# Optimization experiments

Hardware: AMD Instinct MI355X
Metric: run time of the kernel (lower is better)

## Reference

```python
import jax, jax.numpy as jnp
import numpy as np

N = 1024
E = 10
IN = 78
NOTE = 128
BEAT = 64
MEAS = 32
S = NOTE + (BEAT + MEAS) * 2  # 320, GatedGraph state width
SEC = NOTE                    # secondary_size
HEADS = 8
NPB = 4    # notes per beat
BPM = 4    # beats per measure
NB = N // NPB                 # 256 beats
NM = N // (NPB * BPM)         # 64 measures
SEQ_ITER = 2
GRAPH_ITER = 2


def setup_inputs() -> dict:
    key = jax.random.key(0)
    ks = iter(jax.random.split(key, 64))
    def rn(shape, s=0.05):
        return jax.random.normal(next(ks), shape, jnp.float32) * s
    nodes = jax.random.normal(next(ks), (1, N, IN), jnp.float32)
    adjacency = (jax.random.uniform(next(ks), (E, N, N)) < 0.01).astype(jnp.float32)
    beat_numbers = jnp.arange(N, dtype=jnp.int32) // NPB
    measure_numbers = jnp.arange(N, dtype=jnp.int32) // (NPB * BPM)
    inp = dict(nodes=nodes, adjacency=adjacency,
               beat_numbers=beat_numbers, measure_numbers=measure_numbers,
               num_beats=NB, num_measures=NM)
    inp['note_fc_w'] = rn((IN, NOTE)); inp['note_fc_b'] = rn((NOTE,))
    for g in ('g1', 'g2'):
        inp[g+'_wz'] = rn((E, S, SEC)); inp[g+'_wr'] = rn((E, S, SEC)); inp[g+'_wh'] = rn((E, S, SEC))
        inp[g+'_uz'] = rn((SEC, SEC)); inp[g+'_ur'] = rn((SEC, SEC)); inp[g+'_uh'] = rn((SEC, SEC))
        inp[g+'_bz'] = rn((SEC,)); inp[g+'_br'] = rn((SEC,)); inp[g+'_bh'] = rn((SEC,))
    inp['gb_w'] = rn((S, S)); inp['gb_b'] = rn((S,))
    inp['batt_w'] = rn((2*NOTE, 2*NOTE)); inp['batt_b'] = rn((2*NOTE,)); inp['batt_c'] = rn((HEADS, 2*NOTE//HEADS), 1.0)
    inp['matt_w'] = rn((2*BEAT, 2*BEAT)); inp['matt_b'] = rn((2*BEAT,)); inp['matt_c'] = rn((HEADS, 2*BEAT//HEADS), 1.0)
    inp['blstm_wi_f'] = rn((4*BEAT, 2*NOTE)); inp['blstm_wh_f'] = rn((4*BEAT, BEAT)); inp['blstm_b_f'] = rn((4*BEAT,))
    inp['blstm_wi_b'] = rn((4*BEAT, 2*NOTE)); inp['blstm_wh_b'] = rn((4*BEAT, BEAT)); inp['blstm_b_b'] = rn((4*BEAT,))
    inp['mlstm_wi_f'] = rn((4*MEAS, 2*BEAT)); inp['mlstm_wh_f'] = rn((4*MEAS, MEAS)); inp['mlstm_b_f'] = rn((4*MEAS,))
    inp['mlstm_wi_b'] = rn((4*MEAS, 2*BEAT)); inp['mlstm_wh_b'] = rn((4*MEAS, MEAS)); inp['mlstm_b_b'] = rn((4*MEAS,))
    return inp


def gated_graph(x, adj, wz, wr, wh, uz, ur, uh, bz, br, bh, n_iter, sec):
    # x: (N, S); adj: (E, N, N). Faithful to virtuosoNet GatedGraph (batch=1).
    for _ in range(n_iter):
        act = jnp.einsum('emn,mf->enf', adj, x)            # adj[e]^T @ x
        mz = jnp.einsum('enf,efs->ns', act, wz)            # sum over edge types
        mr = jnp.einsum('enf,efs->ns', act, wr)
        mh = jnp.einsum('enf,efs->ns', act, wh)
        xs = x[:, -sec:]
        z = jax.nn.sigmoid(mz + xs @ uz + bz)
        r = jax.nn.sigmoid(mr + xs @ ur + br)
        h = jnp.tanh(mh + (r * xs) @ uh + bh)
        new_sec = (1.0 - z) * xs + r * h                   # virtuosoNet update rule
        x = jnp.concatenate([x[:, :-sec], new_sec], axis=1)
    return x


def seg_attention(x, seg, G, W, b, c):
    # ContextAttention pooled per ragged segment. x: (M, D), c: (H, hd)
    M, D = x.shape
    H, hd = c.shape
    a = jnp.tanh(x @ W + b).reshape(M, H, hd)
    sim = jnp.einsum('mhd,hd->mh', a, c)
    mx = jax.ops.segment_max(sim, seg, num_segments=G)
    w = jnp.exp(sim - mx[seg])
    den = jax.ops.segment_sum(w, seg, num_segments=G)
    w = w / den[seg]
    out = jax.ops.segment_sum(x.reshape(M, H, hd) * w[:, :, None], seg, num_segments=G)
    return out.reshape(G, D)


def lstm_dir(x, wi, wh, b, H):
    def step(carry, xt):
        h, c = carry
        g = wi @ xt + wh @ h + b
        i, f, gg, o = jnp.split(g, 4)
        c = jax.nn.sigmoid(f) * c + jax.nn.sigmoid(i) * jnp.tanh(gg)
        h = jax.nn.sigmoid(o) * jnp.tanh(c)
        return (h, c), h
    init = (jnp.zeros((H,), x.dtype), jnp.zeros((H,), x.dtype))
    _, hs = jax.lax.scan(step, init, x)
    return hs


def bilstm(x, wif, whf, bf, wib, whb, bb, H):
    fw = lstm_dir(x, wif, whf, bf, H)
    bw = lstm_dir(x[::-1], wib, whb, bb, H)[::-1]
    return jnp.concatenate([fw, bw], axis=-1)


def reference(nodes, adjacency, note_fc_w, note_fc_b,
              g1_wz, g1_wr, g1_wh, g1_uz, g1_ur, g1_uh, g1_bz, g1_br, g1_bh,
              gb_w, gb_b,
              g2_wz, g2_wr, g2_wh, g2_uz, g2_ur, g2_uh, g2_bz, g2_br, g2_bh,
              batt_w, batt_b, batt_c, matt_w, matt_b, matt_c,
              blstm_wi_f, blstm_wh_f, blstm_b_f, blstm_wi_b, blstm_wh_b, blstm_b_b,
              mlstm_wi_f, mlstm_wh_f, mlstm_b_f, mlstm_wi_b, mlstm_wh_b, mlstm_b_b,
              beat_numbers, measure_numbers, num_beats, num_measures):
    n = nodes.shape[1]
    x0 = jnp.tanh(nodes[0] @ note_fc_w + note_fc_b)                     # (N, NOTE)
    notes_hidden = jnp.concatenate(
        [jnp.zeros((n, (BEAT + MEAS) * 2), jnp.float32), x0], axis=1)  # (N, S)
    # measure index of each beat = measure at the first note of that beat
    beat_to_meas = jax.ops.segment_min(measure_numbers, beat_numbers, num_segments=num_beats)
    nh2 = notes_hidden
    for _ in range(SEQ_ITER):
        nh = gated_graph(notes_hidden, adjacency, g1_wz, g1_wr, g1_wh,
                         g1_uz, g1_ur, g1_uh, g1_bz, g1_br, g1_bh, GRAPH_ITER, SEC)
        nb = jax.nn.relu(nh @ gb_w + gb_b)
        nh2 = gated_graph(nb, adjacency, g2_wz, g2_wr, g2_wh,
                          g2_uz, g2_ur, g2_uh, g2_bz, g2_br, g2_bh, GRAPH_ITER, SEC)
        cat = jnp.concatenate([nh[:, -SEC:], nh2[:, -SEC:]], axis=-1)   # (N, 2*NOTE)
        beat_nodes = seg_attention(cat, beat_numbers, num_beats, batt_w, batt_b, batt_c)
        beat_hidden = bilstm(beat_nodes, blstm_wi_f, blstm_wh_f, blstm_b_f,
                             blstm_wi_b, blstm_wh_b, blstm_b_b, BEAT)   # (NB, 2*BEAT)
        measure_nodes = seg_attention(beat_hidden, beat_to_meas, num_measures, matt_w, matt_b, matt_c)
        measure_hidden = bilstm(measure_nodes, mlstm_wi_f, mlstm_wh_f, mlstm_b_f,
                                mlstm_wi_b, mlstm_wh_b, mlstm_b_b, MEAS)  # (NM, 2*MEAS)
        beat_spanned = beat_hidden[beat_numbers]                        # (N, 2*BEAT)
        meas_spanned = measure_hidden[measure_numbers]                  # (N, 2*MEAS)
        notes_hidden = jnp.concatenate([beat_spanned, meas_spanned, nh[:, -SEC:]], axis=-1)
    final = jnp.concatenate([notes_hidden, nh2[:, -SEC:]], axis=-1)     # (N, S + NOTE)
    return final[None]  # 'total_note_cat': (1, N, 448)
```

## Files before the change

### kernel.cpp

```cpp
#include <hip/hip_runtime.h>
#include <math.h>


#define NN    1024
#define EE    10
#define INDIM 78
#define SS    320
#define SECD  128
#define NB    256
#define NM    64
#define CAP   64

typedef float v2f __attribute__((ext_vector_type(2)));

__device__ __forceinline__ void pkfma(v2f& a, v2f x, v2f y){
    asm("v_pk_fma_f32 %0, %1, %2, %0" : "+v"(a) : "v"(x), "v"(y));
}
__device__ __forceinline__ void pkfma_blo(v2f& a, v2f x, v2f b){
    asm("v_pk_fma_f32 %0, %1, %2, %0 op_sel:[0,0,0] op_sel_hi:[1,0,1]"
        : "+v"(a) : "v"(x), "v"(b));
}
__device__ __forceinline__ void pkfma_bhi(v2f& a, v2f x, v2f b){
    asm("v_pk_fma_f32 %0, %1, %2, %0 op_sel:[0,1,0] op_sel_hi:[1,1,1]"
        : "+v"(a) : "v"(x), "v"(b));
}

#define LO2(F) ((v2f){F.x, F.y})
#define HI2(F) ((v2f){F.z, F.w})

__device__ __forceinline__ float fsig(float x){
    return __builtin_amdgcn_rcpf(1.f + __expf(-x));
}
__device__ __forceinline__ float ftanh(float x){
    return 1.f - 2.f*__builtin_amdgcn_rcpf(1.f + __expf(2.f*x));
}

__global__ void k_note_fc(const float* __restrict__ nodes, const float* __restrict__ W,
                          const float* __restrict__ b, float* __restrict__ nh){
    int n = blockIdx.x, s = threadIdx.x;
    __shared__ float xrow[INDIM];
    if (s < INDIM) xrow[s] = nodes[n*INDIM + s];
    __syncthreads();
    float acc = b[s];
    for (int k = 0; k < INDIM; ++k) acc += xrow[k]*W[k*128 + s];
    nh[n*SS + 192 + s] = ftanh(acc);
    nh[n*SS + s] = 0.f;
    if (s < 64) nh[n*SS + 128 + s] = 0.f;
}

__global__ void k_csr_build(const float* __restrict__ adj, int* __restrict__ cnt,
                            int* __restrict__ idx){
    int em = blockIdx.x;
    int e = em / NN, m = em % NN;
    const float4* row4 = (const float4*)(adj + (size_t)em * NN);
    int q = threadIdx.x;
    float4 v = row4[q];
    int n0 = q*4;
    if (v.x != 0.f){ int p = atomicAdd(&cnt[e*NN + n0+0], 1); if (p < CAP) idx[((size_t)e*NN + n0+0)*CAP + p] = m; }
    if (v.y != 0.f){ int p = atomicAdd(&cnt[e*NN + n0+1], 1); if (p < CAP) idx[((size_t)e*NN + n0+1)*CAP + p] = m; }
    if (v.z != 0.f){ int p = atomicAdd(&cnt[e*NN + n0+2], 1); if (p < CAP) idx[((size_t)e*NN + n0+2)*CAP + p] = m; }
    if (v.w != 0.f){ int p = atomicAdd(&cnt[e*NN + n0+3], 1); if (p < CAP) idx[((size_t)e*NN + n0+3)*CAP + p] = m; }
}

__global__ void k_gather_full(const float* __restrict__ x, const int* __restrict__ cnt,
                              const int* __restrict__ idx, float* __restrict__ act){
    int en = blockIdx.x*4 + threadIdx.x/80;
    int q  = threadIdx.x % 80;
    int c = cnt[en]; if (c > CAP) c = CAP;
    const int* lst = idx + (size_t)en*CAP;
    float4 acc = {0.f,0.f,0.f,0.f};
    const float* xb = x + q*4;
    for (int j = 0; j < c; ++j){
        float4 v = *(const float4*)(xb + (size_t)lst[j]*SS);
        acc.x += v.x; acc.y += v.y; acc.z += v.z; acc.w += v.w;
    }
    *(float4*)(act + (size_t)en*SS + q*4) = acc;
}

__global__ void k_gather_dyn(const float* __restrict__ x, const int* __restrict__ cnt,
                             const int* __restrict__ idx, float* __restrict__ act){
    int en = blockIdx.x*8 + (threadIdx.x >> 5);
    int q  = threadIdx.x & 31;
    int c = cnt[en]; if (c > CAP) c = CAP;
    const int* lst = idx + (size_t)en*CAP;
    float4 acc = {0.f,0.f,0.f,0.f};
    const float* xb = x + 192 + q*4;
    for (int j = 0; j < c; ++j){
        float4 v = *(const float4*)(xb + (size_t)lst[j]*SS);
        acc.x += v.x; acc.y += v.y; acc.z += v.z; acc.w += v.w;
    }
    *(float4*)(act + (size_t)en*SS + 192 + q*4) = acc;
}

__device__ __forceinline__ void gemm_body(const float* __restrict__ act,
        const float* __restrict__ W, float* __restrict__ outp,
        const float* __restrict__ addv, int K0, int K1, int nt, int z,
        float* A, float* B){
    int tid = threadIdx.x;
    int tx = tid & 31;
    int ty = tid >> 5;
    v2f acc[2][4];
    #pragma unroll
    for (int i=0;i<2;i++)
        #pragma unroll
        for (int j=0;j<4;j++) acc[i][j] = (v2f){0.f,0.f};
    for (int eh = 0; eh < 2; ++eh){
        int e = z*2 + eh;
        const float* Ae = act + (size_t)e*NN*SS + (size_t)nt*32*SS;
        const float* We = W   + (size_t)e*SS*SECD;
        for (int kc = K0; kc < K1; kc += 32){
            {
                int r  = tid >> 3;
                int k4 = (tid & 7) << 2;
                float4 v = *(const float4*)(Ae + r*SS + kc + k4);
                A[(k4+0)*36 + r] = v.x; A[(k4+1)*36 + r] = v.y;
                A[(k4+2)*36 + r] = v.z; A[(k4+3)*36 + r] = v.w;
            }
            #pragma unroll
            for (int i=0;i<4;i++){
                int lin4 = tid + i*256;
                int kk = lin4 >> 5;
                int c4 = (lin4 & 31) << 2;
                *((float4*)(B + kk*132 + c4)) = *(const float4*)(We + (kc+kk)*SECD + c4);
            }
            __syncthreads();
            #pragma unroll 8
            for (int k=0;k<32;k++){
                float4 a4 = *(const float4*)(A + k*36 + ty*4);
                v2f a01 = LO2(a4), a23 = HI2(a4);
                float4 b = *(const float4*)(B + k*132 + tx*4);
                v2f b01 = {b.x, b.y}, b23 = {b.z, b.w};
                pkfma_blo(acc[0][0], a01, b01); pkfma_bhi(acc[0][1], a01, b01);
                pkfma_blo(acc[0][2], a01, b23); pkfma_bhi(acc[0][3], a01, b23);
                pkfma_blo(acc[1][0], a23, b01); pkfma_bhi(acc[1][1], a23, b01);
                pkfma_blo(acc[1][2], a23, b23); pkfma_bhi(acc[1][3], a23, b23);
            }
            __syncthreads();
        }
    }
    size_t base = ((size_t)z*NN + (size_t)nt*32)*384;
    float* P = outp + base;
    int r0 = ty*4;
    float4 o0 = make_float4(acc[0][0].x, acc[0][1].x, acc[0][2].x, acc[0][3].x);
    float4 o1 = make_float4(acc[0][0].y, acc[0][1].y, acc[0][2].y, acc[0][3].y);
    float4 o2 = make_float4(acc[1][0].x, acc[1][1].x, acc[1][2].x, acc[1][3].x);
    float4 o3 = make_float4(acc[1][0].y, acc[1][1].y, acc[1][2].y, acc[1][3].y);
    if (addv){
        const float* Q = addv + base;
        float4 q0 = *(const float4*)(Q + (size_t)(r0+0)*384 + tx*4);
        float4 q1 = *(const float4*)(Q + (size_t)(r0+1)*384 + tx*4);
        float4 q2 = *(const float4*)(Q + (size_t)(r0+2)*384 + tx*4);
        float4 q3 = *(const float4*)(Q + (size_t)(r0+3)*384 + tx*4);
        o0.x+=q0.x; o0.y+=q0.y; o0.z+=q0.z; o0.w+=q0.w;
        o1.x+=q1.x; o1.y+=q1.y; o1.z+=q1.z; o1.w+=q1.w;
        o2.x+=q2.x; o2.y+=q2.y; o2.z+=q2.z; o2.w+=q2.w;
        o3.x+=q3.x; o3.y+=q3.y; o3.z+=q3.z; o3.w+=q3.w;
    }
    *(float4*)(P + (size_t)(r0+0)*384 + tx*4) = o0;
    *(float4*)(P + (size_t)(r0+1)*384 + tx*4) = o1;
    *(float4*)(P + (size_t)(r0+2)*384 + tx*4) = o2;
    *(float4*)(P + (size_t)(r0+3)*384 + tx*4) = o3;
}

__global__ __launch_bounds__(256) void k_gate_gemm_dyn(const float* __restrict__ act,
        const float* __restrict__ wz, const float* __restrict__ wr,
        const float* __restrict__ wh, float* __restrict__ part,
        const float* __restrict__ addv){
    __shared__ float A[32*36];
    __shared__ float B[32*132];
    int g = blockIdx.y;
    const float* W = (g==0) ? wz : ((g==1) ? wr : wh);
    const float* av = addv ? (addv + g*SECD) : nullptr;
    gemm_body(act, W, part + g*SECD, av, 192, 320, blockIdx.x, blockIdx.z, A, B);
}

__global__ __launch_bounds__(256) void k_gate_gemm_both(const float* __restrict__ act,
        const float* __restrict__ wz, const float* __restrict__ wr,
        const float* __restrict__ wh, float* __restrict__ part,
        float* __restrict__ part_s){
    __shared__ float A[32*36];
    __shared__ float B[32*132];
    int y = blockIdx.y;
    int g = (y >= 3) ? (y - 3) : y;
    const float* W = (g==0) ? wz : ((g==1) ? wr : wh);
    if (y >= 3)
        gemm_body(act, W, part   + g*SECD, nullptr, 192, 320, blockIdx.x, blockIdx.z, A, B);
    else
        gemm_body(act, W, part_s + g*SECD, nullptr,   0, 192, blockIdx.x, blockIdx.z, A, B);
}

__global__ __launch_bounds__(256) void k_gru(float* __restrict__ x,
        const float* __restrict__ part, int nsp,
        const float* __restrict__ uz, const float* __restrict__ ur, const float* __restrict__ uh,
        const float* __restrict__ bz, const float* __restrict__ br, const float* __restrict__ bh){
    int n0 = blockIdx.x*2;
    int tid = threadIdx.x;
    int s = tid & 127;
    int h = tid >> 7;
    int k0 = h*64;
    __shared__ float xs[2][SECD], rx[2][SECD];
    __shared__ float red[2][2][2][SECD];
    if (h == 0){
        xs[0][s] = x[(n0+0)*SS + 192 + s];
        xs[1][s] = x[(n0+1)*SS + 192 + s];
    }
    __syncthreads();
    float mz[2]={0,0}, mr[2]={0,0}, mh[2]={0,0};
    if (h == 0){
        for (int sp=0; sp<nsp; sp++){
            const float* Pp = part + ((size_t)sp*NN + n0)*384;
            #pragma unroll
            for (int j=0;j<2;j++){
                mz[j] += Pp[j*384 + s];
                mr[j] += Pp[j*384 + 128 + s];
                mh[j] += Pp[j*384 + 256 + s];
            }
        }
    }
    float dz[2]={0,0}, dr[2]={0,0};
    #pragma unroll 8
    for (int k=k0;k<k0+64;k++){
        float wz_ = uz[k*SECD + s], wr_ = ur[k*SECD + s];
        #pragma unroll
        for (int j=0;j<2;j++){ float xv = xs[j][k]; dz[j] += xv*wz_; dr[j] += xv*wr_; }
    }
    red[0][h][0][s]=dz[0]; red[0][h][1][s]=dz[1];
    red[1][h][0][s]=dr[0]; red[1][h][1][s]=dr[1];
    __syncthreads();
    float zz[2], rr[2];
    if (h == 0){
        #pragma unroll
        for (int j=0;j<2;j++){
            float dzf = red[0][0][j][s] + red[0][1][j][s];
            float drf = red[1][0][j][s] + red[1][1][j][s];
            zz[j] = fsig(mz[j] + dzf + bz[s]);
            rr[j] = fsig(mr[j] + drf + br[s]);
            rx[j][s] = rr[j]*xs[j][s];
        }
    }
    __syncthreads();
    float dh[2]={0,0};
    #pragma unroll 8
    for (int k=k0;k<k0+64;k++){
        float wh_ = uh[k*SECD + s];
        #pragma unroll
        for (int j=0;j<2;j++) dh[j] += rx[j][k]*wh_;
    }
    red[0][h][0][s]=dh[0]; red[0][h][1][s]=dh[1];
    __syncthreads();
    if (h == 0){
        #pragma unroll
        for (int j=0;j<2;j++){
            float dhf = red[0][0][j][s] + red[0][1][j][s];
            float hc = ftanh(mh[j] + dhf + bh[s]);
            x[(n0+j)*SS + 192 + s] = (1.f - zz[j])*xs[j][s] + rr[j]*hc;
        }
    }
}

__global__ __launch_bounds__(640) void k_gb(const float* __restrict__ nh,
                     const float* __restrict__ W,
                     const float* __restrict__ b, float* __restrict__ nb){
    int n0 = blockIdx.x*4;
    int tid = threadIdx.x;
    int h = (tid >= 320) ? 1 : 0;
    int s = tid - h*320;
    int k0 = h*160;
    __shared__ float xr_t[SS*4];
    __shared__ float red[2][4][SS];
    if (h == 0){
        float v0 = nh[(n0+0)*SS + s], v1 = nh[(n0+1)*SS + s];
        float v2 = nh[(n0+2)*SS + s], v3 = nh[(n0+3)*SS + s];
        *(float4*)(xr_t + s*4) = make_float4(v0,v1,v2,v3);
    }
    __syncthreads();
    v2f a01={0.f,0.f}, a23={0.f,0.f};
    #pragma unroll 8
    for (int k=k0;k<k0+160;k++){
        float wv = W[k*SS + s];
        v2f ws = {wv, wv};
        const v2f* xp = (const v2f*)(xr_t + k*4);
        pkfma(a01, xp[0], ws);
        pkfma(a23, xp[1], ws);
    }
    red[h][0][s]=a01.x; red[h][1][s]=a01.y; red[h][2][s]=a23.x; red[h][3][s]=a23.y;
    __syncthreads();
    if (h == 0){
        float bv = b[s];
        nb[(n0+0)*SS + s] = fmaxf(bv + red[0][0][s] + red[1][0][s], 0.f);
        nb[(n0+1)*SS + s] = fmaxf(bv + red[0][1][s] + red[1][1][s], 0.f);
        nb[(n0+2)*SS + s] = fmaxf(bv + red[0][2][s] + red[1][2][s], 0.f);
        nb[(n0+3)*SS + s] = fmaxf(bv + red[0][3][s] + red[1][3][s], 0.f);
    }
}

__global__ __launch_bounds__(512) void k_batt_fused(
        const float* __restrict__ nh, const float* __restrict__ nh2,
        const float* __restrict__ W, const float* __restrict__ b,
        const float* __restrict__ cvec,
        const float* __restrict__ wi_f, const float* __restrict__ b_f,
        const float* __restrict__ wi_b, const float* __restrict__ b_b,
        float* __restrict__ gf, float* __restrict__ gbo){
    int g = blockIdx.x;
    int tid = threadIdx.x;
    int s = tid & 255;
    int h = tid >> 8;
    __shared__ float xr_t[256*4];
    __shared__ float simw[4][8];
    __shared__ float wgt[4][8];
    __shared__ float bnode[256];
    __shared__ float red[2][4][256];
    if (h == 0){
        float c0,c1,c2,c3;
        if (s < 128){
            c0 = nh[(g*4+0)*SS + 192 + s]; c1 = nh[(g*4+1)*SS + 192 + s];
            c2 = nh[(g*4+2)*SS + 192 + s]; c3 = nh[(g*4+3)*SS + 192 + s];
        } else {
            c0 = nh2[(g*4+0)*SS + 64 + s]; c1 = nh2[(g*4+1)*SS + 64 + s];
            c2 = nh2[(g*4+2)*SS + 64 + s]; c3 = nh2[(g*4+3)*SS + 64 + s];
        }
        *(float4*)(xr_t + s*4) = make_float4(c0,c1,c2,c3);
    }
    __syncthreads();
    {
        int k0 = h*128;
        v2f ac01 = {0.f,0.f}, ac23 = {0.f,0.f};
        #pragma unroll 8
        for (int k=k0;k<k0+128;k++){
            float wv = W[k*256 + s];
            v2f ws = {wv, wv};
            const v2f* xp = (const v2f*)(xr_t + k*4);
            pkfma(ac01, xp[0], ws);
            pkfma(ac23, xp[1], ws);
        }
        red[h][0][s]=ac01.x; red[h][1][s]=ac01.y; red[h][2][s]=ac23.x; red[h][3][s]=ac23.y;
    }
    __syncthreads();
    int hd = s >> 5;
    if (h == 0){
        float bias = b[s];
        float cv = cvec[s];
        #pragma unroll
        for (int j=0;j<4;j++){
            float p = ftanh(bias + red[0][j][s] + red[1][j][s])*cv;
            #pragma unroll
            for (int off=16; off>0; off>>=1) p += __shfl_down(p, off);
            if ((s & 31) == 0) simw[j][hd] = p;
        }
    }
    __syncthreads();
    if (tid < 8){
        float v0=simw[0][tid], v1=simw[1][tid], v2=simw[2][tid], v3=simw[3][tid];
        float mx = fmaxf(fmaxf(v0,v1), fmaxf(v2,v3));
        float e0=__expf(v0-mx), e1=__expf(v1-mx), e2=__expf(v2-mx), e3=__expf(v3-mx);
        float den = e0+e1+e2+e3;
        wgt[0][tid]=e0/den; wgt[1][tid]=e1/den; wgt[2][tid]=e2/den; wgt[3][tid]=e3/den;
    }
    __syncthreads();
    if (h == 0){
        float4 xs4 = *(const float4*)(xr_t + s*4);
        bnode[s] = xs4.x*wgt[0][hd] + xs4.y*wgt[1][hd] + xs4.z*wgt[2][hd] + xs4.w*wgt[3][hd];
    }
    __syncthreads();
    {
        v2f afA = {0.f,0.f}, afB = {0.f,0.f};
        v2f abA = {0.f,0.f}, abB = {0.f,0.f};
        const v2f* wfp = (const v2f*)(wi_f + (size_t)s*256);
        const v2f* wbp = (const v2f*)(wi_b + (size_t)s*256);
        const v2f* bp  = (const v2f*)bnode;
        int q0 = h*64;
        #pragma unroll 8
        for (int k2=q0;k2<q0+64;k2+=2){
            v2f x01 = bp[k2], x23 = bp[k2+1];
            pkfma(afA, wfp[k2], x01); pkfma(afB, wfp[k2+1], x23);
            pkfma(abA, wbp[k2], x01); pkfma(abB, wbp[k2+1], x23);
        }
        red[h][0][s] = (afA.x + afA.y) + (afB.x + afB.y);
        red[h][1][s] = (abA.x + abA.y) + (abB.x + abB.y);
    }
    __syncthreads();
    if (h == 0){
        gf [g*256 + s] = b_f[s] + red[0][0][s] + red[1][0][s];
        gbo[g*256 + s] = b_b[s] + red[0][1][s] + red[1][1][s];
    }
}

__global__ __launch_bounds__(256) void k_matt_fused(
        const float* __restrict__ bh,
        const float* __restrict__ W, const float* __restrict__ b,
        const float* __restrict__ cvec,
        const float* __restrict__ wi_f, const float* __restrict__ b_f,
        const float* __restrict__ wi_b, const float* __restrict__ b_b,
        float* __restrict__ gf, float* __restrict__ gbo){
    int g = blockIdx.x;
    int tid = threadIdx.x;
    int s = tid & 127;
    int h = tid >> 7;
    __shared__ float xr_t[128*4];
    __shared__ float simw[4][8];
    __shared__ float wgt[4][8];
    __shared__ float mnode[128];
    __shared__ float red[2][4][128];
    if (h == 0){
        float c0 = bh[(g*4+0)*128 + s], c1 = bh[(g*4+1)*128 + s];
        float c2 = bh[(g*4+2)*128 + s], c3 = bh[(g*4+3)*128 + s];
        *(float4*)(xr_t + s*4) = make_float4(c0,c1,c2,c3);
    }
    __syncthreads();
    {
        int k0 = h*64;
        v2f ac01 = {0.f,0.f}, ac23 = {0.f,0.f};
        #pragma unroll 8
        for (int k=k0;k<k0+64;k++){
            float wv = W[k*128 + s];
            v2f ws = {wv, wv};
            const v2f* xp = (const v2f*)(xr_t + k*4);
            pkfma(ac01, xp[0], ws);
            pkfma(ac23, xp[1], ws);
        }
        red[h][0][s]=ac01.x; red[h][1][s]=ac01.y; red[h][2][s]=ac23.x; red[h][3][s]=ac23.y;
    }
    __syncthreads();
    int hd = s >> 4;
    if (h == 0){
        float bias = b[s];
        float cv = cvec[s];
        #pragma unroll
        for (int j=0;j<4;j++){
            float p = ftanh(bias + red[0][j][s] + red[1][j][s])*cv;
            #pragma unroll
            for (int off=8; off>0; off>>=1) p += __shfl_down(p, off);
            if ((s & 15) == 0) simw[j][hd] = p;
        }
    }
    __syncthreads();
    if (tid < 8){
        float v0=simw[0][tid], v1=simw[1][tid], v2=simw[2][tid], v3=simw[3][tid];
        float mx = fmaxf(fmaxf(v0,v1), fmaxf(v2,v3));
        float e0=__expf(v0-mx), e1=__expf(v1-mx), e2=__expf(v2-mx), e3=__expf(v3-mx);
        float den = e0+e1+e2+e3;
        wgt[0][tid]=e0/den; wgt[1][tid]=e1/den; wgt[2][tid]=e2/den; wgt[3][tid]=e3/den;
    }
    __syncthreads();
    if (h == 0){
        float4 xs4 = *(const float4*)(xr_t + s*4);
        mnode[s] = xs4.x*wgt[0][hd] + xs4.y*wgt[1][hd] + xs4.z*wgt[2][hd] + xs4.w*wgt[3][hd];
    }
    __syncthreads();
    {
        v2f afA = {0.f,0.f}, afB = {0.f,0.f};
        v2f abA = {0.f,0.f}, abB = {0.f,0.f};
        const v2f* wfp = (const v2f*)(wi_f + (size_t)s*128);
        const v2f* wbp = (const v2f*)(wi_b + (size_t)s*128);
        const v2f* bp  = (const v2f*)mnode;
        int q0 = h*32;
        #pragma unroll 8
        for (int k2=q0;k2<q0+32;k2+=2){
            v2f x01 = bp[k2], x23 = bp[k2+1];
            pkfma(afA, wfp[k2], x01); pkfma(afB, wfp[k2+1], x23);
            pkfma(abA, wbp[k2], x01); pkfma(abB, wbp[k2+1], x23);
        }
        red[h][0][s] = (afA.x + afA.y) + (afB.x + afB.y);
        red[h][1][s] = (abA.x + abA.y) + (abB.x + abB.y);
    }
    __syncthreads();
    if (h == 0){
        gf [g*128 + s] = b_f[s] + red[0][0][s] + red[1][0][s];
        gbo[g*128 + s] = b_b[s] + red[0][1][s] + red[1][1][s];
    }
}

__global__ __launch_bounds__(256)
__attribute__((amdgpu_waves_per_eu(1, 1)))
void k_lstm_rec64(
        const float* __restrict__ gin_f, const float* __restrict__ wh_f,
        const float* __restrict__ gin_b, const float* __restrict__ wh_b,
        float* __restrict__ hid ){
    const int H = 64, T = 256;
    int dir = blockIdx.x;
    const float* gin = dir ? gin_b : gin_f;
    const float* wh  = dir ? wh_b  : wh_f;
    int gi = threadIdx.x;
    int w  = gi >> 6;
    int j  = gi & 63;
    int o  = j & 15;
    int g  = j >> 4;
    int l  = (w << 4) + o;
    int row = (g << 6) + l;
    const v2f* wp = (const v2f*)(wh + (size_t)row*H);
    v2f w00=wp[0], w01=wp[1], w02=wp[2], w03=wp[3], w04=wp[4], w05=wp[5], w06=wp[6], w07=wp[7],
        w08=wp[8], w09=wp[9], w10=wp[10],w11=wp[11],w12=wp[12],w13=wp[13],w14=wp[14],w15=wp[15],
        w16=wp[16],w17=wp[17],w18=wp[18],w19=wp[19],w20=wp[20],w21=wp[21],w22=wp[22],w23=wp[23],
        w24=wp[24],w25=wp[25],w26=wp[26],w27=wp[27],w28=wp[28],w29=wp[29],w30=wp[30],w31=wp[31];
    __shared__ __align__(16) float hsb[2][H];
    float c = 0.f;
    if (gi < H) hsb[0][gi] = 0.f;
    __syncthreads();
    const float* gp = gin + row;
    float gcur = gp[(dir ? (T-1) : 0)*256];
    for (int step=0; step<T; step++){
        int t = dir ? (T-1-step) : step;
        float gnext = 0.f;
        if (step+1 < T) gnext = gp[(dir ? (T-2-step) : (step+1))*256];
        const float4* hv = (const float4*)hsb[step & 1];
        float4 H0=hv[0],  H1=hv[1],  H2=hv[2],  H3=hv[3];
        float4 H4=hv[4],  H5=hv[5],  H6=hv[6],  H7=hv[7];
        float4 H8=hv[8],  H9=hv[9],  H10=hv[10],H11=hv[11];
        float4 H12=hv[12],H13=hv[13],H14=hv[14],H15=hv[15];
        v2f A0={gcur,0.f}, A1={0.f,0.f}, A2={0.f,0.f}, A3={0.f,0.f};
        pkfma(A0,w00,LO2(H0));  pkfma(A1,w01,HI2(H0));  pkfma(A2,w02,LO2(H1));  pkfma(A3,w03,HI2(H1));
        pkfma(A0,w04,LO2(H2));  pkfma(A1,w05,HI2(H2));  pkfma(A2,w06,LO2(H3));  pkfma(A3,w07,HI2(H3));
        pkfma(A0,w08,LO2(H4));  pkfma(A1,w09,HI2(H4));  pkfma(A2,w10,LO2(H5));  pkfma(A3,w11,HI2(H5));
        pkfma(A0,w12,LO2(H6));  pkfma(A1,w13,HI2(H6));  pkfma(A2,w14,LO2(H7));  pkfma(A3,w15,HI2(H7));
        pkfma(A0,w16,LO2(H8));  pkfma(A1,w17,HI2(H8));  pkfma(A2,w18,LO2(H9));  pkfma(A3,w19,HI2(H9));
        pkfma(A0,w20,LO2(H10)); pkfma(A1,w21,HI2(H10)); pkfma(A2,w22,LO2(H11)); pkfma(A3,w23,HI2(H11));
        pkfma(A0,w24,LO2(H12)); pkfma(A1,w25,HI2(H12)); pkfma(A2,w26,LO2(H13)); pkfma(A3,w27,HI2(H13));
        pkfma(A0,w28,LO2(H14)); pkfma(A1,w29,HI2(H14)); pkfma(A2,w30,LO2(H15)); pkfma(A3,w31,HI2(H15));
        float val = ((A0.x+A0.y) + (A1.x+A1.y)) + ((A2.x+A2.y) + (A3.x+A3.y));
        float i_ = __shfl(val, o);
        float f_ = __shfl(val, o + 16);
        float g_ = __shfl(val, o + 32);
        float o_ = __shfl(val, o + 48);
        c = fsig(f_)*c + fsig(i_)*ftanh(g_);
        float hn = fsig(o_)*ftanh(c);
        if (g == 0){
            hsb[(step+1)&1][l] = hn;
            hid[t*2*H + dir*H + l] = hn;
        }
        __syncthreads();
        gcur = gnext;
    }
}

__global__ __launch_bounds__(64)
__attribute__((amdgpu_waves_per_eu(1, 1)))
void k_lstm_rec32(
        const float* __restrict__ gin_f, const float* __restrict__ wh_f,
        const float* __restrict__ gin_b, const float* __restrict__ wh_b,
        float* __restrict__ hid ){
    const int H = 32, T = 64;
    int dir = blockIdx.x;
    const float* gin = dir ? gin_b : gin_f;
    const float* wh  = dir ? wh_b  : wh_f;
    int gi = threadIdx.x;
    v2f wA[16], wB[16];
    {
        const v2f* rA = (const v2f*)(wh + (size_t)(     gi)*H);
        const v2f* rB = (const v2f*)(wh + (size_t)(64 + gi)*H);
        #pragma unroll
        for (int k=0;k<16;k++){ wA[k]=rA[k]; wB[k]=rB[k]; }
    }
    __shared__ __align__(16) float hs[H];
    float c = 0.f;
    if (gi < H) hs[gi] = 0.f;
    __syncthreads();
    const float* gp = gin + gi;
    int ts0 = dir ? (T-1) : 0, ts1 = dir ? (T-2) : 1;
    float g0 = gp[ts0*128], g1 = gp[ts0*128 + 64];
    float n0 = gp[ts1*128], n1 = gp[ts1*128 + 64];
    bool lo = (gi < H);
    for (int step=0; step<T; step++){
        int t = dir ? (T-1-step) : step;
        float p0=0.f, p1=0.f;
        if (step+2 < T){
            int tp = dir ? (T-3-step) : (step+2);
            p0 = gp[tp*128]; p1 = gp[tp*128 + 64];
        }
        v2f aA = {g0, 0.f}, aB = {g1, 0.f};
        const float4* hv = (const float4*)hs;
        #pragma unroll
        for (int k=0;k<8;k++){
            float4 h4 = hv[k];
            pkfma(aA, wA[2*k],   LO2(h4));
            pkfma(aB, wB[2*k],   LO2(h4));
            pkfma(aA, wA[2*k+1], HI2(h4));
            pkfma(aB, wB[2*k+1], HI2(h4));
        }
        float sA = aA.x + aA.y;
        float sB = aB.x + aB.y;
        float pA = __shfl(sA, gi ^ 32);
        float pB = __shfl(sB, gi ^ 32);
        float i_ = lo ? sA : pA;
        float f_ = lo ? pA : sA;
        float g_ = lo ? sB : pB;
        float o_ = lo ? pB : sB;
        c = fsig(f_)*c + fsig(i_)*ftanh(g_);
        float hn = fsig(o_)*ftanh(c);
        if (lo){
            hid[t*2*H + dir*H + gi] = hn;
            hs[gi] = hn;
        }
        g0 = n0; g1 = n1; n0 = p0; n1 = p1;
    }
}

__global__ void k_spans(float* __restrict__ nh, const float* __restrict__ bh,
                        const float* __restrict__ mh,
                        const int* __restrict__ bn, const int* __restrict__ mn){
    int n = blockIdx.x, s = threadIdx.x;
    float v;
    if (s < 128)      v = bh[bn[n]*128 + s];
    else if (s < 192) v = mh[mn[n]*64 + (s-128)];
    else              v = nh[n*SS + s];
    nh[n*SS + s] = v;
}

__global__ void k_spans_out(const float* __restrict__ bh, const float* __restrict__ mh,
                            const float* __restrict__ nh, const float* __restrict__ nh2,
                            const int* __restrict__ bn, const int* __restrict__ mn,
                            float* __restrict__ out){
    int n = blockIdx.x, s = threadIdx.x;
    float v;
    if (s < 128)      v = bh[bn[n]*128 + s];
    else if (s < 192) v = mh[mn[n]*64 + (s-128)];
    else if (s < 320) v = nh[n*SS + s];
    else              v = nh2[n*SS + 192 + (s-320)];
    out[n*448 + s] = v;
}

extern "C" void kernel_launch(void* const* d_in, const int* in_sizes, int n_in,
                              void* d_out, int out_size, void* d_ws, size_t ws_size,
                              hipStream_t stream) {
    const float* nodes    = (const float*)d_in[0];
    const float* adj      = (const float*)d_in[1];
    const int*   bn       = (const int*)  d_in[2];
    const int*   mn       = (const int*)  d_in[3];
    const float* fc_w     = (const float*)d_in[6];
    const float* fc_b     = (const float*)d_in[7];
    const float* g_wz[2]  = {(const float*)d_in[8],  (const float*)d_in[17]};
    const float* g_wr[2]  = {(const float*)d_in[9],  (const float*)d_in[18]};
    const float* g_wh[2]  = {(const float*)d_in[10], (const float*)d_in[19]};
    const float* g_uz[2]  = {(const float*)d_in[11], (const float*)d_in[20]};
    const float* g_ur[2]  = {(const float*)d_in[12], (const float*)d_in[21]};
    const float* g_uh[2]  = {(const float*)d_in[13], (const float*)d_in[22]};
    const float* g_bz[2]  = {(const float*)d_in[14], (const float*)d_in[23]};
    const float* g_br[2]  = {(const float*)d_in[15], (const float*)d_in[24]};
    const float* g_bh[2]  = {(const float*)d_in[16], (const float*)d_in[25]};
    const float* gb_w     = (const float*)d_in[26];
    const float* gb_b     = (const float*)d_in[27];
    const float* batt_w   = (const float*)d_in[28];
    const float* batt_b   = (const float*)d_in[29];
    const float* batt_c   = (const float*)d_in[30];
    const float* matt_w   = (const float*)d_in[31];
    const float* matt_b   = (const float*)d_in[32];
    const float* matt_c   = (const float*)d_in[33];
    const float* bwi_f    = (const float*)d_in[34];
    const float* bwh_f    = (const float*)d_in[35];
    const float* bb_f     = (const float*)d_in[36];
    const float* bwi_b    = (const float*)d_in[37];
    const float* bwh_b    = (const float*)d_in[38];
    const float* bb_b     = (const float*)d_in[39];
    const float* mwi_f    = (const float*)d_in[40];
    const float* mwh_f    = (const float*)d_in[41];
    const float* mb_f     = (const float*)d_in[42];
    const float* mwi_b    = (const float*)d_in[43];
    const float* mwh_b    = (const float*)d_in[44];
    const float* mb_b     = (const float*)d_in[45];
    float* out = (float*)d_out;

    float* W_   = (float*)d_ws;
    float* nh   = W_;
    float* nh2  = nh   + 327680;
    float* act  = nh2  + 327680;
    float* part = act  + 3276800;
    float* bgf  = part + 3932160;
    float* bgb  = bgf  + 65536;
    float* beat_hidden = bgb + 65536;
    float* mgf  = beat_hidden + 32768;
    float* mgb  = mgf  + 8192;
    float* meas_hidden = mgb + 8192;
    int*   cnt  = (int*)(meas_hidden + 4096);
    int*   idx  = cnt + 10240;

    float* part_s = part + 5*NN*384;

    hipMemsetAsync(cnt, 0, EE*NN*sizeof(int), stream);
    k_csr_build<<<EE*NN, 256, 0, stream>>>(adj, cnt, idx);
    k_note_fc<<<NN, 128, 0, stream>>>(nodes, fc_w, fc_b, nh);

    for (int si = 0; si < 2; ++si){
        for (int half = 0; half < 2; ++half){
            float* x = half ? nh2 : nh;
            int w = half;
            bool zerostatic = (si == 0 && half == 0);
            if (half == 1)
                k_gb<<<NN/4, 640, 0, stream>>>(nh, gb_w, gb_b, nh2);
            for (int it = 0; it < 2; ++it){
                if (!zerostatic && it == 0){
                    k_gather_full<<<EE*NN/4, 320, 0, stream>>>(x, cnt, idx, act);
                    k_gate_gemm_both<<<dim3(32,6,5), 256, 0, stream>>>(
                            act, g_wz[w], g_wr[w], g_wh[w], part, part_s);
                } else {
                    k_gather_dyn<<<EE*NN/8, 256, 0, stream>>>(x, cnt, idx, act);
                    k_gate_gemm_dyn<<<dim3(32,3,5), 256, 0, stream>>>(
                            act, g_wz[w], g_wr[w], g_wh[w], part,
                            zerostatic ? nullptr : part_s);
                }
                int nsp = (!zerostatic && it == 0) ? 10 : 5;
                k_gru<<<NN/2, 256, 0, stream>>>(x, part, nsp,
                        g_uz[w], g_ur[w], g_uh[w], g_bz[w], g_br[w], g_bh[w]);
            }
        }
        k_batt_fused<<<NB, 512, 0, stream>>>(nh, nh2, batt_w, batt_b, batt_c,
                                             bwi_f, bb_f, bwi_b, bb_b, bgf, bgb);
        k_lstm_rec64<<<2, 256, 0, stream>>>(bgf, bwh_f, bgb, bwh_b, beat_hidden);
        k_matt_fused<<<NM, 256, 0, stream>>>(beat_hidden, matt_w, matt_b, matt_c,
                                             mwi_f, mb_f, mwi_b, mb_b, mgf, mgb);
        k_lstm_rec32<<<2, 64, 0, stream>>>(mgf, mwh_f, mgb, mwh_b, meas_hidden);
        if (si == 0)
            k_spans<<<NN, SS, 0, stream>>>(nh, beat_hidden, meas_hidden, bn, mn);
        else
            k_spans_out<<<NN, 448, 0, stream>>>(beat_hidden, meas_hidden, nh, nh2,
                                                bn, mn, out);
    }
}
```

Measured before the change: 970.8 us.

## Load GEMM weight tiles directly to LDS and widen GRU block to 512 threads

The gate GEMM now fills its weight tile with global_load_lds, which writes global memory straight into LDS instead of staging it through registers. The tile drops its padding, so the row stride goes from 132 to 128 floats. The GRU kernel doubles its threads: the recurrent matvecs are split four ways over k, and two extra thread groups sum the partial products in parallel with them. This aims to cut register traffic in the GEMM and the serial partial-sum latency in the GRU, at the cost of more shared memory and an extra reduction step.

New measurement: 952.1 us. Within noise of the previous version (-1.9%).

```diff
diff --git a/kernel.cpp b/kernel.cpp
--- a/kernel.cpp
+++ b/kernel.cpp
@@ -119,16 +119,18 @@
             #pragma unroll
             for (int i=0;i<4;i++){
                 int lin4 = tid + i*256;
-                int kk = lin4 >> 5;
-                int c4 = (lin4 & 31) << 2;
-                *((float4*)(B + kk*132 + c4)) = *(const float4*)(We + (kc+kk)*SECD + c4);
+                __builtin_amdgcn_global_load_lds(
+                    (const __attribute__((address_space(1))) unsigned int*)
+                        (We + (size_t)kc*SECD + (size_t)lin4*4),
+                    (__attribute__((address_space(3))) unsigned int*)(B + lin4*4),
+                    16, 0, 0);
             }
             __syncthreads();
             #pragma unroll 8
             for (int k=0;k<32;k++){
                 float4 a4 = *(const float4*)(A + k*36 + ty*4);
                 v2f a01 = LO2(a4), a23 = HI2(a4);
-                float4 b = *(const float4*)(B + k*132 + tx*4);
+                float4 b = *(const float4*)(B + k*128 + tx*4);
                 v2f b01 = {b.x, b.y}, b23 = {b.z, b.w};
                 pkfma_blo(acc[0][0], a01, b01); pkfma_bhi(acc[0][1], a01, b01);
                 pkfma_blo(acc[0][2], a01, b23); pkfma_bhi(acc[0][3], a01, b23);
@@ -167,7 +169,7 @@
         const float* __restrict__ wh, float* __restrict__ part,
         const float* __restrict__ addv){
     __shared__ float A[32*36];
-    __shared__ float B[32*132];
+    __shared__ float B[32*128];
     int g = blockIdx.y;
     const float* W = (g==0) ? wz : ((g==1) ? wr : wh);
     const float* av = addv ? (addv + g*SECD) : nullptr;
@@ -179,7 +181,7 @@
         const float* __restrict__ wh, float* __restrict__ part,
         float* __restrict__ part_s){
     __shared__ float A[32*36];
-    __shared__ float B[32*132];
+    __shared__ float B[32*128];
     int y = blockIdx.y;
     int g = (y >= 3) ? (y - 3) : y;
     const float* W = (g==0) ? wz : ((g==1) ? wr : wh);
@@ -189,25 +191,25 @@
         gemm_body(act, W, part_s + g*SECD, nullptr,   0, 192, blockIdx.x, blockIdx.z, A, B);
 }
 
-__global__ __launch_bounds__(256) void k_gru(float* __restrict__ x,
+__global__ __launch_bounds__(512) void k_gru(float* __restrict__ x,
         const float* __restrict__ part, int nsp,
         const float* __restrict__ uz, const float* __restrict__ ur, const float* __restrict__ uh,
         const float* __restrict__ bz, const float* __restrict__ br, const float* __restrict__ bh){
     int n0 = blockIdx.x*2;
     int tid = threadIdx.x;
-    int s = tid & 127;
-    int h = tid >> 7;
-    int k0 = h*64;
+    int s  = tid & 127;
+    int qh = tid >> 7;
+    int k0 = qh*32;
     __shared__ float xs[2][SECD], rx[2][SECD];
-    __shared__ float red[2][2][2][SECD];
-    if (h == 0){
+    __shared__ float redz[4][2][SECD], redr[4][2][SECD];
+    __shared__ float redm[2][3][2][SECD];
+    if (qh == 0){
         xs[0][s] = x[(n0+0)*SS + 192 + s];
         xs[1][s] = x[(n0+1)*SS + 192 + s];
     }
-    __syncthreads();
-    float mz[2]={0,0}, mr[2]={0,0}, mh[2]={0,0};
-    if (h == 0){
-        for (int sp=0; sp<nsp; sp++){
+    if (qh >= 2){
+        float mz[2]={0,0}, mr[2]={0,0}, mh[2]={0,0};
+        for (int sp = qh-2; sp < nsp; sp += 2){
             const float* Pp = part + ((size_t)sp*NN + n0)*384;
             #pragma unroll
             for (int j=0;j<2;j++){
@@ -216,43 +218,51 @@
                 mh[j] += Pp[j*384 + 256 + s];
             }
         }
-    }
+        int hh = qh - 2;
+        redm[hh][0][0][s]=mz[0]; redm[hh][0][1][s]=mz[1];
+        redm[hh][1][0][s]=mr[0]; redm[hh][1][1][s]=mr[1];
+        redm[hh][2][0][s]=mh[0]; redm[hh][2][1][s]=mh[1];
+    }
+    __syncthreads();
     float dz[2]={0,0}, dr[2]={0,0};
     #pragma unroll 8
-    for (int k=k0;k<k0+64;k++){
+    for (int k=k0;k<k0+32;k++){
         float wz_ = uz[k*SECD + s], wr_ = ur[k*SECD + s];
         #pragma unroll
         for (int j=0;j<2;j++){ float xv = xs[j][k]; dz[j] += xv*wz_; dr[j] += xv*wr_; }
     }
-    red[0][h][0][s]=dz[0]; red[0][h][1][s]=dz[1];
-    red[1][h][0][s]=dr[0]; red[1][h][1][s]=dr[1];
+    redz[qh][0][s]=dz[0]; redz[qh][1][s]=dz[1];
+    redr[qh][0][s]=dr[0]; redr[qh][1][s]=dr[1];
     __syncthreads();
     float zz[2], rr[2];
-    if (h == 0){
+    if (qh == 0){
         #pragma unroll
         for (int j=0;j<2;j++){
-            float dzf = red[0][0][j][s] + red[0][1][j][s];
-            float drf = red[1][0][j][s] + red[1][1][j][s];
-            zz[j] = fsig(mz[j] + dzf + bz[s]);
-            rr[j] = fsig(mr[j] + drf + br[s]);
+            float mzf = redm[0][0][j][s] + redm[1][0][j][s];
+            float mrf = redm[0][1][j][s] + redm[1][1][j][s];
+            float dzf = (redz[0][j][s]+redz[1][j][s]) + (redz[2][j][s]+redz[3][j][s]);
+            float drf = (redr[0][j][s]+redr[1][j][s]) + (redr[2][j][s]+redr[3][j][s]);
+            zz[j] = fsig(mzf + dzf + bz[s]);
+            rr[j] = fsig(mrf + drf + br[s]);
             rx[j][s] = rr[j]*xs[j][s];
         }
     }
     __syncthreads();
     float dh[2]={0,0};
     #pragma unroll 8
-    for (int k=k0;k<k0+64;k++){
+    for (int k=k0;k<k0+32;k++){
         float wh_ = uh[k*SECD + s];
         #pragma unroll
         for (int j=0;j<2;j++) dh[j] += rx[j][k]*wh_;
     }
-    red[0][h][0][s]=dh[0]; red[0][h][1][s]=dh[1];
-    __syncthreads();
-    if (h == 0){
+    redz[qh][0][s]=dh[0]; redz[qh][1][s]=dh[1];
+    __syncthreads();
+    if (qh == 0){
         #pragma unroll
         for (int j=0;j<2;j++){
-            float dhf = red[0][0][j][s] + red[0][1][j][s];
-            float hc = ftanh(mh[j] + dhf + bh[s]);
+            float mhf = redm[0][2][j][s] + redm[1][2][j][s];
+            float dhf = (redz[0][j][s]+redz[1][j][s]) + (redz[2][j][s]+redz[3][j][s]);
+            float hc = ftanh(mhf + dhf + bh[s]);
             x[(n0+j)*SS + 192 + s] = (1.f - zz[j])*xs[j][s] + rr[j]*hc;
         }
     }
@@ -697,7 +707,7 @@
                             zerostatic ? nullptr : part_s);
                 }
                 int nsp = (!zerostatic && it == 0) ? 10 : 5;
-                k_gru<<<NN/2, 256, 0, stream>>>(x, part, nsp,
+                k_gru<<<NN/2, 512, 0, stream>>>(x, part, nsp,
                         g_uz[w], g_ur[w], g_uh[w], g_bz[w], g_br[w], g_bh[w]);
             }
         }
```
